# Kernel optimization log

Hardware: AMD Instinct MI355X
Metric: run time of the kernel (lower is better)

## Reference

```python
import jax, jax.numpy as jnp
import numpy as np
from jax import lax


def _l2n(t, eps=1e-12):
    n = jnp.sqrt(jnp.sum(t * t, axis=-1, keepdims=True))
    return t / jnp.maximum(n, eps)


def _ln(t, w, b, eps=1e-5):
    mu = jnp.mean(t, -1, keepdims=True)
    var = jnp.var(t, -1, keepdims=True)
    return (t - mu) / jnp.sqrt(var + eps) * w + b


def _unfold3(x):
    # nn.Unfold(kernel_size=3, padding=1, stride=1): [B,C,H,W] -> [B,C,9,H*W]
    B, C, H, W = x.shape
    xp = jnp.pad(x, ((0, 0), (0, 0), (1, 1), (1, 1)))
    pat = jnp.stack([xp[:, :, i:i + H, j:j + W] for i in range(3) for j in range(3)], axis=2)
    return pat.reshape(B, C, 9, H * W)


def _forward(x, norm1_w, norm1_b, q_w, q_b, kv_w, kv_b, temperature, query_embedding,
             learnable_tokens, learnable_bias, sr_w, sr_b, pln_w, pln_b, proj_w, proj_b,
             norm2_w, norm2_b, fc1_w, fc1_b, dw_w, dw_b, fc2_w, fc2_b):
    B, C, H, W = x.shape
    nh = temperature.shape[0]
    d = C // nh
    N = H * W
    K = 9  # local_len = window_size**2
    # norm1 (WithBias LayerNorm over channel dim, channels-last)
    y = _ln(x.reshape(B, C, N).transpose(0, 2, 1), norm1_w, norm1_b)  # [B,N,C]
    # ---- AggregatedAttention ----
    q = (y @ q_w.T + q_b).reshape(B, N, nh, d).transpose(0, 2, 1, 3)  # [B,h,N,d]
    qn = _l2n(q)
    qs = (qn + query_embedding) * jax.nn.softplus(temperature)
    kv = y @ kv_w.T + kv_b  # [B,N,2C]
    k_loc = _l2n(kv[..., :C].reshape(B, N, nh, d)).reshape(B, N, C)
    kvl = jnp.concatenate([k_loc, kv[..., C:]], -1).transpose(0, 2, 1).reshape(B, 2 * C, H, W)
    pat = _unfold3(kvl).reshape(B, 2 * nh, d, K, N).transpose(0, 1, 4, 2, 3)  # [B,2h,N,d,K]
    k_l, v_l = pat[:, :nh], pat[:, nh:]
    attn_local = jnp.einsum('bhnd,bhndk->bhnk', qs, k_l)  # [B,h,N,K]
    # pooled branch; sr_ratio=1 so adaptive_avg_pool2d is identity
    y4 = y.transpose(0, 2, 1).reshape(B, C, H, W)
    xp = jax.nn.gelu(jnp.einsum('oc,bchw->bohw', sr_w, y4) + sr_b[:, None, None], approximate=False)
    xp = _ln(xp.reshape(B, C, N).transpose(0, 2, 1), pln_w, pln_b)  # [B,pool_len,C]
    kvp = (xp @ kv_w.T + kv_b).reshape(B, N, 2 * nh, d).transpose(0, 2, 1, 3)
    k_p = _l2n(kvp[:, :nh])
    v_p = kvp[:, nh:]
    attn_pool = jnp.einsum('bhnd,bhmd->bhnm', qs, k_p)  # [B,h,N,pool_len]
    attn = jax.nn.softmax(jnp.concatenate([attn_local, attn_pool], -1), axis=-1)
    a_l, a_p = attn[..., :K], attn[..., K:]
    w_l = jnp.einsum('bhnd,hdk->bhnk', qn, learnable_tokens) + learnable_bias + a_l
    x_local = jnp.einsum('bhnk,bhndk->bhnd', w_l, v_l)
    x_pool = jnp.einsum('bhnm,bhmd->bhnd', a_p, v_p)
    xo = (x_local + x_pool).transpose(0, 2, 1, 3).reshape(B, N, C)
    # proj then raw torch-style reshape [B,N,C] -> [B,C,H,W] (memory reinterpretation)
    xo = (xo @ proj_w.T + proj_b).reshape(B, C, H, W)
    x = x + xo
    # ---- ConvolutionalGLU MLP ----
    hf = dw_b.shape[0]
    y2 = _ln(x.reshape(B, C, N).transpose(0, 2, 1), norm2_w, norm2_b).transpose(0, 2, 1).reshape(B, C, H, W)
    f1 = jnp.einsum('oc,bchw->bohw', fc1_w, y2) + fc1_b[:, None, None]
    a, v = f1[:, :hf], f1[:, hf:]
    dw = lax.conv_general_dilated(a, dw_w, (1, 1), ((1, 1), (1, 1)),
                                  feature_group_count=hf,
                                  dimension_numbers=('NCHW', 'OIHW', 'NCHW')) + dw_b[:, None, None]
    g = jax.nn.gelu(dw, approximate=False) * v
    out = jnp.einsum('oc,bchw->bohw', fc2_w, g) + fc2_b[:, None, None]
    return x + out


def setup_inputs() -> dict:
    key = jax.random.key(0)
    B, C, H, W = 2, 128, 56, 56
    nh, d, K = 4, 32, 9
    hf = int(2 * int(C * 4.0) / 3)  # 341
    ks = iter(jax.random.split(key, 16))
    rn = lambda shape, s=0.02: jax.random.normal(next(ks), shape, jnp.float32) * s
    return {
        'x': jax.random.normal(next(ks), (B, C, H, W), jnp.float32),
        'norm1_w': jnp.ones((C,), jnp.float32), 'norm1_b': jnp.zeros((C,), jnp.float32),
        'q_w': rn((C, C)), 'q_b': jnp.zeros((C,), jnp.float32),
        'kv_w': rn((2 * C, C)), 'kv_b': jnp.zeros((2 * C,), jnp.float32),
        'temperature': jnp.full((nh, 1, 1), float(np.log(np.exp(1.0 / 0.24) - 1.0)), jnp.float32),
        'query_embedding': rn((nh, 1, d)),
        'learnable_tokens': rn((nh, d, K)),
        'learnable_bias': jnp.zeros((nh, 1, K), jnp.float32),
        'sr_w': rn((C, C)), 'sr_b': jnp.zeros((C,), jnp.float32),
        'pln_w': jnp.ones((C,), jnp.float32), 'pln_b': jnp.zeros((C,), jnp.float32),
        'proj_w': rn((C, C)), 'proj_b': jnp.zeros((C,), jnp.float32),
        'norm2_w': jnp.ones((C,), jnp.float32), 'norm2_b': jnp.zeros((C,), jnp.float32),
        'fc1_w': rn((2 * hf, C)), 'fc1_b': jnp.zeros((2 * hf,), jnp.float32),
        'dw_w': rn((hf, 1, 3, 3)), 'dw_b': jnp.zeros((hf,), jnp.float32),
        'fc2_w': rn((C, hf)), 'fc2_b': jnp.zeros((C,), jnp.float32),
    }


def reference(x, norm1_w, norm1_b, q_w, q_b, kv_w, kv_b, temperature, query_embedding,
              learnable_tokens, learnable_bias, sr_w, sr_b, pln_w, pln_b, proj_w, proj_b,
              norm2_w, norm2_b, fc1_w, fc1_b, dw_w, dw_b, fc2_w, fc2_b):
    return _forward(x, norm1_w, norm1_b, q_w, q_b, kv_w, kv_b, temperature, query_embedding,
                    learnable_tokens, learnable_bias, sr_w, sr_b, pln_w, pln_b, proj_w, proj_b,
                    norm2_w, norm2_b, fc1_w, fc1_b, dw_w, dw_b, fc2_w, fc2_b)
```

## Files before the change

### kernel.cpp

```cpp
#include <hip/hip_runtime.h>
#include <hip/hip_bf16.h>

typedef __hip_bfloat16 bf16;
typedef _Float16 f16;
typedef short s8v __attribute__((ext_vector_type(8)));
typedef short s4v __attribute__((ext_vector_type(4)));
typedef float f4v __attribute__((ext_vector_type(4)));

#define DEVI __device__ __forceinline__

DEVI float cvt(float x){ return x; }
DEVI float cvt(bf16 x){ return __bfloat162float(x); }

DEVI void stg(float* p, float v){ *p = v; }
DEVI void stg(bf16* p, float v){ *p = __float2bfloat16(v); }

DEVI float gelu_exact(float x){
  return 0.5f*x*(1.0f + erff(x*0.70710678118654752440f));
}

constexpr int B_ = 2, C_ = 128, H_ = 56, W_ = 56, N_ = 3136, NH_ = 4, D_ = 32, HF_ = 341;
constexpr int ROWS_ = B_*N_;
constexpr int KF2 = 352;
constexpr int GQ_ = NH_*B_*N_;
constexpr int FW = 512;
constexpr int KSP = 8;
constexpr int SPLIT = 384;
constexpr float LOG2E = 1.4426950408889634f;
constexpr float E8L2  = 11.541560327111707f;

template<typename TX, typename TY, bool PLANES>
__global__ __launch_bounds__(256)
void ln_kernel(const TX* __restrict__ x, long xstr, const float* __restrict__ w,
               const float* __restrict__ bia, TY* __restrict__ y)
{
  int gid = blockIdx.x*4 + (threadIdx.x>>6);
  int lane = threadIdx.x & 63;
  int b = gid / N_, n = gid % N_;
  float v0, v1;
  if (PLANES){
    v0 = cvt(x[((long)b*C_ + lane     )*N_ + n]);
    v1 = cvt(x[((long)b*C_ + lane + 64)*N_ + n]);
  } else {
    v0 = cvt(x[(long)gid*xstr + lane     ]);
    v1 = cvt(x[(long)gid*xstr + lane + 64]);
  }
  float s = v0+v1, ss = v0*v0 + v1*v1;
  #pragma unroll
  for (int o=32;o>0;o>>=1){ s += __shfl_xor(s,o); ss += __shfl_xor(ss,o); }
  float mu  = s*(1.0f/128.0f);
  float var = fmaxf(ss*(1.0f/128.0f) - mu*mu, 0.f);
  float inv = rsqrtf(var + 1e-5f);
  stg(&y[(long)gid*C_ + lane     ], (v0-mu)*inv*w[lane     ] + bia[lane     ]);
  stg(&y[(long)gid*C_ + lane + 64], (v1-mu)*inv*w[lane + 64] + bia[lane + 64]);
}

__global__ __launch_bounds__(256)
void head_kernel(const float* __restrict__ q_w, const float* __restrict__ kv_w,
                 const float* __restrict__ sr_w, const float* __restrict__ proj_w,
                 const float* __restrict__ fc1_w, const float* __restrict__ fc2_w,
                 const float* __restrict__ q_b, const float* __restrict__ kv_b,
                 const float* __restrict__ sr_b,
                 bf16* __restrict__ out, float* __restrict__ bias_out,
                 const float* __restrict__ x_in, const float* __restrict__ n1w,
                 const float* __restrict__ n1b, bf16* __restrict__ y)
{
  if (blockIdx.x >= 839){
    int gid = (blockIdx.x - 839)*4 + (threadIdx.x>>6);
    int lane = threadIdx.x & 63;
    int b = gid / N_, n = gid % N_;
    float v0 = x_in[((long)b*C_ + lane     )*N_ + n];
    float v1 = x_in[((long)b*C_ + lane + 64)*N_ + n];
    float s = v0+v1, ss = v0*v0 + v1*v1;
    #pragma unroll
    for (int o=32;o>0;o>>=1){ s += __shfl_xor(s,o); ss += __shfl_xor(ss,o); }
    float mu  = s*(1.0f/128.0f);
    float var = fmaxf(ss*(1.0f/128.0f) - mu*mu, 0.f);
    float inv = rsqrtf(var + 1e-5f);
    y[(long)gid*C_ + lane     ] = __float2bfloat16((v0-mu)*inv*n1w[lane     ] + n1b[lane     ]);
    y[(long)gid*C_ + lane + 64] = __float2bfloat16((v1-mu)*inv*n1w[lane + 64] + n1b[lane + 64]);
    return;
  }
  int t = blockIdx.x*256 + threadIdx.x;
  if (t >= 214272){
    int i = t - 214272;
    if (i < 512){
      float bv = (i < 128) ? q_b[i] : (i < 384) ? kv_b[i-128] : sr_b[i-384];
      bias_out[i] = bv;
    }
    return;
  }
  float v;
  if      (t <  16384) v = q_w[t];
  else if (t <  49152) v = kv_w[t-16384];
  else if (t <  65536) v = sr_w[t-49152];
  else if (t <  81920) v = proj_w[t-65536];
  else if (t < 169216) v = fc1_w[t-81920];
  else {
    int i = t - 169216; int m = i / KF2, kp = i % KF2;
    v = (kp < HF_) ? fc2_w[m*HF_ + kp] : 0.f;
  }
  out[t] = __float2bfloat16(v);
}

template<int KT, int MODE, typename TC, int BM=64>
__global__ __launch_bounds__(256)
void gemm_mfma(const bf16* __restrict__ A, const bf16* __restrict__ B,
               const float* __restrict__ bias, const float* __restrict__ res,
               TC* __restrict__ Cm, int M, int Nn,
               long sA, long sB, long sC, long sR,
               const float* __restrict__ qe, const float* __restrict__ temp,
               bf16* __restrict__ aux0, bf16* __restrict__ aux1)
{
  A  += (long)blockIdx.z * sA;
  B  += (long)blockIdx.z * sB;
  Cm += (long)blockIdx.z * sC;
  if (res) res += (long)blockIdx.z * sR;
  int lane = threadIdx.x & 63, w = threadIdx.x >> 6;
  int m = lane & 15, quad = lane >> 4;
  int n0 = blockIdx.x*64, m0 = blockIdx.y*BM;
  int arow = m0 + w*16 + m;
  if (arow >= M) arow = M-1;
  const bf16* ap = A + (long)arow*KT + quad*8;
  const bf16* bp = B + (long)(n0 + m)*KT + quad*8;
  f4v acc[4];
  #pragma unroll
  for (int s=0;s<4;s++) acc[s] = (f4v){0.f,0.f,0.f,0.f};
  #pragma unroll
  for (int k0 = 0; k0 < KT; k0 += 32){
    s8v af = *(const s8v*)(ap + k0);
    #pragma unroll
    for (int s=0;s<4;s++){
      s8v bf = *(const s8v*)(bp + (long)s*16*KT + k0);
      acc[s] = __builtin_amdgcn_mfma_f32_16x16x32_bf16(af, bf, acc[s], 0, 0, 0);
    }
  }
  if ((MODE==6 || MODE==7) && blockIdx.x < 2){
    int hA = blockIdx.x*2, hB = hA+1;
    float spA = 0.f, spB = 0.f;
    if (MODE==6){
      spA = log1pf(expf(temp[hA])) * LOG2E;
      spB = log1pf(expf(temp[hB])) * LOG2E;
    }
    #pragma unroll
    for (int r=0;r<4;r++){
      float v4[4];
      #pragma unroll
      for (int s=0;s<4;s++) v4[s] = acc[s][r] + bias[n0 + s*16 + m];
      float ssA = v4[0]*v4[0] + v4[1]*v4[1];
      float ssB = v4[2]*v4[2] + v4[3]*v4[3];
      #pragma unroll
      for (int off=1; off<16; off<<=1){
        ssA += __shfl_xor(ssA, off);
        ssB += __shfl_xor(ssB, off);
      }
      float invA = 1.f/fmaxf(sqrtf(ssA), 1e-12f);
      float invB = 1.f/fmaxf(sqrtf(ssB), 1e-12f);
      int gm = m0 + w*16 + quad*4 + r;
      int b = gm / N_, n = gm % N_;
      #pragma unroll
      for (int s=0;s<4;s++){
        int h = (s<2) ? hA : hB;
        int d = (s&1)*16 + m;
        float v = v4[s] * ((s<2) ? invA : invB);
        if (MODE==6) v = (v + qe[h*D_ + d]) * ((s<2) ? spA : spB);
        aux0[((long)(b*NH_+h)*N_ + n)*D_ + d] = __float2bfloat16(v);
      }
    }
    return;
  }
  if (MODE==7){
    int gm0 = m0 + w*16 + quad*4;
    int b = gm0 / N_, nb = gm0 % N_;
    #pragma unroll
    for (int s=0;s<4;s++){
      int h = (blockIdx.x-2)*2 + (s>>1);
      int d = (s&1)*16 + m;
      bf16 p4[4];
      #pragma unroll
      for (int r=0;r<4;r++) p4[r] = __float2bfloat16(acc[s][r] + bias[n0 + s*16 + m]);
      *(s4v*)(aux1 + ((long)(b*NH_+h)*D_ + d)*N_ + nb) = *(const s4v*)p4;
    }
    return;
  }
  #pragma unroll
  for (int s=0;s<4;s++){
    int gn = n0 + s*16 + m;
    #pragma unroll
    for (int r=0;r<4;r++){
      int gm = m0 + w*16 + quad*4 + r;
      if (gm >= M) continue;
      float v = acc[s][r];
      if (MODE==1 || MODE==4 || MODE==6) v += bias[gn];
      else                               v += bias[gm];
      if (MODE==6 && gn >= 384) v = gelu_exact(v);
      if (MODE==4 || MODE==5) v += res[(long)gm*Nn + gn];
      stg(&Cm[(long)gm*Nn + gn], v);
    }
  }
}

__global__ __launch_bounds__(256)
void attn_part_kernel(const bf16* __restrict__ qs_, const bf16* __restrict__ kp_,
                      const bf16* __restrict__ vp_,
                      bf16* __restrict__ Op, float* __restrict__ Lp)
{
  int bh = blockIdx.y;
  int z  = blockIdx.z;
  int lane = threadIdx.x & 63;
  int w    = threadIdx.x >> 6;
  int m    = lane & 15, quad = lane >> 4;
  int base = blockIdx.x*256 + w*16;
  __shared__ float sm[4][640];
  float* Olds = sm[w];

  s8v af[4]; bool hasQ[4];
  #pragma unroll
  for (int ch=0; ch<4; ch++){
    int qq = base + ch*64;
    hasQ[ch] = (qq < N_);
    af[ch] = *(const s8v*)(qs_ + ((long)bh*N_ + (hasQ[ch] ? qq : base) + m)*D_ + quad*8);
  }
  const bf16* kpb = kp_ + (long)bh*N_*D_;
  const bf16* vpb = vp_ + (long)bh*D_*N_;
  int kperm = (m & 3) + 8*(m >> 2);
  f4v o0[4], o1[4];
  float l[4];
  #pragma unroll
  for (int ch=0; ch<4; ch++){
    o0[ch] = (f4v){0.f,0.f,0.f,0.f}; o1[ch] = (f4v){0.f,0.f,0.f,0.f};
    l[ch] = 0.f;
  }

  int tlo = z*SPLIT, thi = (z==KSP-1) ? N_ : tlo + SPLIT;
  for (int t0 = tlo; t0 < thi; t0 += 64){
    s8v kf[4];
    kf[0] = *(const s8v*)(kpb + (long)(t0 + kperm     )*D_ + quad*8);
    kf[1] = *(const s8v*)(kpb + (long)(t0 + kperm +  4)*D_ + quad*8);
    kf[2] = *(const s8v*)(kpb + (long)(t0 + kperm + 32)*D_ + quad*8);
    kf[3] = *(const s8v*)(kpb + (long)(t0 + kperm + 36)*D_ + quad*8);
    s8v vf0[2], vf1[2];
    #pragma unroll
    for (int c2=0;c2<2;c2++){
      vf0[c2] = *(const s8v*)(vpb + (long)(m     )*N_ + t0 + c2*32 + quad*8);
      vf1[c2] = *(const s8v*)(vpb + (long)(16 + m)*N_ + t0 + c2*32 + quad*8);
    }
    #pragma unroll
    for (int ch=0; ch<4; ch++){
      f4v c[4];
      #pragma unroll
      for (int s=0;s<4;s++){
        c[s] = (f4v){-E8L2, -E8L2, -E8L2, -E8L2};
        c[s] = __builtin_amdgcn_mfma_f32_16x16x32_bf16(kf[s], af[ch], c[s], 0, 0, 0);
      }
      bf16 p8a[8], p8b[8];
      float ls = 0.f;
      #pragma unroll
      for (int r=0;r<4;r++){
        float ea = __builtin_amdgcn_exp2f(c[0][r]);
        float eb = __builtin_amdgcn_exp2f(c[1][r]);
        float ec = __builtin_amdgcn_exp2f(c[2][r]);
        float ed = __builtin_amdgcn_exp2f(c[3][r]);
        ls += (ea+eb) + (ec+ed);
        p8a[r] = __float2bfloat16(ea); p8a[4+r] = __float2bfloat16(eb);
        p8b[r] = __float2bfloat16(ec); p8b[4+r] = __float2bfloat16(ed);
      }
      l[ch] += ls;
      s8v pa = *(const s8v*)p8a, pb = *(const s8v*)p8b;
      o0[ch] = __builtin_amdgcn_mfma_f32_16x16x32_bf16(pa, vf0[0], o0[ch], 0, 0, 0);
      o1[ch] = __builtin_amdgcn_mfma_f32_16x16x32_bf16(pa, vf1[0], o1[ch], 0, 0, 0);
      o0[ch] = __builtin_amdgcn_mfma_f32_16x16x32_bf16(pb, vf0[1], o0[ch], 0, 0, 0);
      o1[ch] = __builtin_amdgcn_mfma_f32_16x16x32_bf16(pb, vf1[1], o1[ch], 0, 0, 0);
    }
  }
  #pragma unroll
  for (int ch=0; ch<4; ch++){
    if (!hasQ[ch]) continue;
    float lr = l[ch];
    lr += __shfl_xor(lr, 16);
    lr += __shfl_xor(lr, 32);
    #pragma unroll
    for (int r=0;r<4;r++){
      Olds[(quad*4+r)*36 + m     ] = o0[ch][r];
      Olds[(quad*4+r)*36 + 16 + m] = o1[ch][r];
    }
    long gq = (long)bh*N_ + base + ch*64 + m;
    f4v ov0 = *(const f4v*)(Olds + m*36 + quad*8);
    f4v ov1 = *(const f4v*)(Olds + m*36 + quad*8 + 4);
    bf16 o8[8];
    #pragma unroll
    for (int j=0;j<4;j++){ o8[j] = __float2bfloat16(ov0[j]); o8[4+j] = __float2bfloat16(ov1[j]); }
    *(s8v*)(Op + ((long)z*GQ_ + gq)*32 + quad*8) = *(const s8v*)o8;
    if (quad == 0) Lp[(long)z*GQ_ + gq] = lr;
  }
}

__global__ __launch_bounds__(256)
void attn_combine_kernel(const bf16* __restrict__ Op, const float* __restrict__ Lp,
                         const bf16* __restrict__ qs_, const bf16* __restrict__ fused,
                         const float* __restrict__ qe, const float* __restrict__ temp,
                         const float* __restrict__ tokens, const float* __restrict__ tbias,
                         bf16* __restrict__ xo)
{
  int t  = blockIdx.x*256 + threadIdx.x;
  int gq = t >> 3;
  int l8 = t & 7;
  int d0 = l8*4;
  int n = gq % N_; int bh = gq / N_; int h = bh & 3; int b = bh >> 2;
  float out[4] = {0.f,0.f,0.f,0.f};
  #pragma unroll
  for (int z=0; z<KSP; z++){
    s4v o4 = *(const s4v*)(Op + ((long)z*GQ_ + gq)*32 + d0);
    #pragma unroll
    for (int j=0;j<4;j++) out[j] += cvt(((const bf16*)&o4)[j]);
  }
  float L = 0.f;
  for (int z=l8; z<KSP; z+=8) L += Lp[(long)z*GQ_ + gq];
  #pragma unroll
  for (int off=1; off<8; off<<=1) L += __shfl_xor(L, off);
  float q[4];
  {
    s4v q4 = *(const s4v*)(qs_ + (long)gq*D_ + d0);
    #pragma unroll
    for (int j=0;j<4;j++) q[j] = cvt(((const bf16*)&q4)[j]) * 0.6931471805599453f;
  }
  int hy = n / W_, wx = n % W_;
  const bf16* kvb = fused + (long)b*N_*FW + 128 + h*D_ + d0;
  float sl[9];
  #pragma unroll
  for (int k=0;k<9;k++){
    int di = k/3-1, dj = k%3-1;
    int yy = hy+di, xx = wx+dj;
    bool ok = (yy>=0 && yy<H_ && xx>=0 && xx<W_);
    float dot = 0.f, ss = 0.f;
    if (ok){
      s4v k4 = *(const s4v*)(kvb + (long)(yy*W_+xx)*FW);
      #pragma unroll
      for (int j=0;j<4;j++){
        float kk = cvt(((const bf16*)&k4)[j]);
        dot = fmaf(q[j], kk, dot);
        ss  = fmaf(kk, kk, ss);
      }
    }
    #pragma unroll
    for (int off=1; off<8; off<<=1){
      dot += __shfl_xor(dot, off);
      ss  += __shfl_xor(ss,  off);
    }
    sl[k] = ok ? dot / fmaxf(sqrtf(ss), 1e-12f) : 0.f;
  }
  #pragma unroll
  for (int k=0;k<9;k++) L += __expf(sl[k] - 8.f);
  float invL = 1.f/L;
  #pragma unroll
  for (int j=0;j<4;j++) out[j] *= invL;
  float sp = log1pf(expf(temp[h]));
  float invsp = 1.f/sp;
  float qn[4];
  #pragma unroll
  for (int j=0;j<4;j++) qn[j] = q[j]*invsp - qe[h*D_ + d0 + j];
  #pragma unroll
  for (int k=0;k<9;k++){
    float tok = 0.f;
    #pragma unroll
    for (int j=0;j<4;j++) tok = fmaf(qn[j], tokens[(h*D_ + d0 + j)*9 + k], tok);
    #pragma unroll
    for (int off=1; off<8; off<<=1) tok += __shfl_xor(tok, off);
    float wl = tok + tbias[h*9+k] + __expf(sl[k] - 8.f)*invL;
    int di = k/3-1, dj = k%3-1;
    int yy = hy+di, xx = wx+dj;
    if (yy>=0 && yy<H_ && xx>=0 && xx<W_){
      s4v v4 = *(const s4v*)(kvb + (long)(yy*W_+xx)*FW + 128);
      #pragma unroll
      for (int j=0;j<4;j++) out[j] = fmaf(wl, cvt(((const bf16*)&v4)[j]), out[j]);
    }
  }
  bf16 o4[4];
  #pragma unroll
  for (int j=0;j<4;j++) o4[j] = __float2bfloat16(out[j]);
  *(s4v*)(xo + ((long)(b*N_ + n))*C_ + h*D_ + d0) = *(const s4v*)o4;
}

__global__ __launch_bounds__(256)
void dwconv_kernel(const bf16* __restrict__ f1, const float* __restrict__ dww,
                   const float* __restrict__ dwb, bf16* __restrict__ g)
{
  int t = blockIdx.x*256 + threadIdx.x;
  if (t >= B_*N_*44) return;
  int b = t / (N_*44); int r = t - b*(N_*44);
  int n = r % N_, cg = r / N_;
  f1 += (long)b*2*HF_*N_;
  g  += (long)b*N_*KF2;
  int c0 = cg*8;
  int hy = n / W_, wx = n % W_;
  bf16 o8[8];
  #pragma unroll
  for (int j=0;j<8;j++){
    int c = c0 + j;
    float val = 0.f;
    if (c < HF_){
      const bf16* ap = f1 + (long)c*N_;
      float s = dwb[c];
      #pragma unroll
      for (int di=-1; di<=1; di++)
        #pragma unroll
        for (int dj=-1; dj<=1; dj++){
          int yy = hy+di, xx = wx+dj;
          if (yy>=0 && yy<H_ && xx>=0 && xx<W_)
            s = fmaf(dww[c*9 + (di+1)*3 + (dj+1)], cvt(ap[yy*W_+xx]), s);
        }
      val = gelu_exact(s) * cvt(f1[(long)(HF_+c)*N_ + n]);
    }
    o8[j] = __float2bfloat16(val);
  }
  *(s8v*)(g + (long)n*KF2 + c0) = *(const s8v*)o8;
}

extern "C" void kernel_launch(void* const* d_in, const int* in_sizes, int n_in,
                              void* d_out, int out_size, void* d_ws, size_t ws_size,
                              hipStream_t stream)
{
  (void)in_sizes; (void)n_in; (void)out_size; (void)ws_size;
  const float* x_in      = (const float*)d_in[0];
  const float* norm1_w   = (const float*)d_in[1];
  const float* norm1_b   = (const float*)d_in[2];
  const float* q_w       = (const float*)d_in[3];
  const float* q_b       = (const float*)d_in[4];
  const float* kv_w      = (const float*)d_in[5];
  const float* kv_b      = (const float*)d_in[6];
  const float* temp      = (const float*)d_in[7];
  const float* qe        = (const float*)d_in[8];
  const float* tokens    = (const float*)d_in[9];
  const float* tbias     = (const float*)d_in[10];
  const float* sr_w      = (const float*)d_in[11];
  const float* sr_b      = (const float*)d_in[12];
  const float* pln_w     = (const float*)d_in[13];
  const float* pln_b     = (const float*)d_in[14];
  const float* proj_w    = (const float*)d_in[15];
  const float* proj_b    = (const float*)d_in[16];
  const float* norm2_w   = (const float*)d_in[17];
  const float* norm2_b   = (const float*)d_in[18];
  const float* fc1_w     = (const float*)d_in[19];
  const float* fc1_b     = (const float*)d_in[20];
  const float* dw_w      = (const float*)d_in[21];
  const float* dw_b      = (const float*)d_in[22];
  const float* fc2_w     = (const float*)d_in[23];
  const float* fc2_b     = (const float*)d_in[24];

  char* w8 = (char*)d_ws;
  bf16*  fused   = (bf16*)(w8 + 0);
  float* x2      = (float*)(w8 + 0);
  bf16*  y2      = (bf16*)(w8 + 3211264);
  bf16*  f1b     = (bf16*)(w8 + 4816896);
  bf16*  qs      = (bf16*)(w8 + 6422528);
  bf16*  xp      = (bf16*)(w8 + 8028160);
  bf16*  k_p     = (bf16*)(w8 + 9633792);
  bf16*  v_p     = (bf16*)(w8 + 11239424);
  bf16*  Opart   = (bf16*)(w8 + 13045056);
  bf16*  g_rows  = (bf16*)(w8 + 32312640);
  bf16*  wbase   = (bf16*)(w8 + 36728128);
  float* fbias   = (float*)(w8 + 37156672);
  bf16*  y       = f1b;
  bf16*  xo      = (bf16*)d_out;
  float* Lpart   = (float*)((char*)d_out + 1605632);
  bf16*  proj_wb = wbase + 65536;
  bf16*  fc1_wb  = wbase + 81920;
  bf16*  fc2_wb  = wbase + 169216;

  head_kernel<<<839 + ROWS_/4, 256, 0, stream>>>(
      q_w, kv_w, sr_w, proj_w, fc1_w, fc2_w, q_b, kv_b, sr_b, wbase, fbias,
      x_in, norm1_w, norm1_b, y);
  gemm_mfma<128, 6, bf16><<<dim3(8,98), 256, 0, stream>>>(
      y, wbase, fbias, nullptr, fused, ROWS_, FW, 0,0,0,0, qe, temp, qs, nullptr);
  ln_kernel<bf16, bf16, false><<<ROWS_/4, 256, 0, stream>>>(fused + 384, FW, pln_w, pln_b, xp);
  gemm_mfma<128, 7, bf16><<<dim3(4,98), 256, 0, stream>>>(
      xp, wbase + 16384, kv_b, nullptr, (bf16*)nullptr, ROWS_, 256, 0,0,0,0,
      nullptr, nullptr, k_p, v_p);
  attn_part_kernel<<<dim3(13,8,KSP), 256, 0, stream>>>(qs, k_p, v_p, Opart, Lpart);
  attn_combine_kernel<<<GQ_*8/256, 256, 0, stream>>>(Opart, Lpart, qs, fused,
                                                     qe, temp, tokens, tbias, xo);
  gemm_mfma<128, 4, float, 32><<<dim3(2,196), 128, 0, stream>>>(
      xo, proj_wb, proj_b, x_in, x2, ROWS_, 128, 0,0,0,0, nullptr, nullptr, nullptr, nullptr);
  ln_kernel<float, bf16, true><<<ROWS_/4, 256, 0, stream>>>(x2, 0, norm2_w, norm2_b, y2);
  gemm_mfma<128, 3, bf16><<<dim3(49,11,B_), 256, 0, stream>>>(
      fc1_wb, y2, fc1_b, nullptr, f1b, 2*HF_, N_,
      0, (long)N_*C_, (long)2*HF_*N_, 0, nullptr, nullptr, nullptr, nullptr);
  dwconv_kernel<<<(B_*N_*44+255)/256, 256, 0, stream>>>(f1b, dw_w, dw_b, g_rows);
  gemm_mfma<KF2, 5, float, 32><<<dim3(49,4,B_), 128, 0, stream>>>(
      fc2_wb, g_rows, fc2_b, x2, (float*)d_out, C_, N_,
      0, (long)N_*KF2, (long)C_*N_, (long)C_*N_, nullptr, nullptr, nullptr, nullptr);
}
```

Before: 245.6 us.

## Fuse pooled LayerNorm into kv GEMM and double-buffer K/V loads in attention

The separate LayerNorm kernel over the pooled branch is removed. Each MODE-7 GEMM lane now loads its A row from the fused buffer with stride FW, computes the row mean and variance with cross-lane shuffles, and normalizes in registers before the MFMA loop. The attention partial kernel also gets a two-stage register double buffer that loads the next K/V tile while the current one is computed. This saves a launch and an intermediate round trip through memory, but raises register pressure and recomputes the LayerNorm for every column block.

```diff
diff --git a/kernel.cpp b/kernel.cpp
--- a/kernel.cpp
+++ b/kernel.cpp
@@ -2,7 +2,6 @@
 #include <hip/hip_bf16.h>
 
 typedef __hip_bfloat16 bf16;
-typedef _Float16 f16;
 typedef short s8v __attribute__((ext_vector_type(8)));
 typedef short s4v __attribute__((ext_vector_type(4)));
 typedef float f4v __attribute__((ext_vector_type(4)));
@@ -103,7 +102,7 @@
   out[t] = __float2bfloat16(v);
 }
 
-template<int KT, int MODE, typename TC, int BM=64>
+template<int KT, int MODE, typename TC, int BM=64, int LDA=KT>
 __global__ __launch_bounds__(256)
 void gemm_mfma(const bf16* __restrict__ A, const bf16* __restrict__ B,
                const float* __restrict__ bias, const float* __restrict__ res,
@@ -121,14 +120,41 @@
   int n0 = blockIdx.x*64, m0 = blockIdx.y*BM;
   int arow = m0 + w*16 + m;
   if (arow >= M) arow = M-1;
-  const bf16* ap = A + (long)arow*KT + quad*8;
+  const bf16* ap = A + (long)arow*LDA + quad*8;
   const bf16* bp = B + (long)(n0 + m)*KT + quad*8;
+  s8v a4[KT/32];
+  if (MODE==7){
+    float s=0.f, ssum=0.f;
+    #pragma unroll
+    for (int i=0;i<KT/32;i++){
+      a4[i] = *(const s8v*)(ap + i*32);
+      #pragma unroll
+      for (int j=0;j<8;j++){
+        float v = cvt(((const bf16*)&a4[i])[j]);
+        s += v; ssum = fmaf(v,v,ssum);
+      }
+    }
+    s    += __shfl_xor(s,16);    s    += __shfl_xor(s,32);
+    ssum += __shfl_xor(ssum,16); ssum += __shfl_xor(ssum,32);
+    float mu  = s*(1.0f/128.0f);
+    float var = fmaxf(ssum*(1.0f/128.0f) - mu*mu, 0.f);
+    float inv = rsqrtf(var + 1e-5f);
+    #pragma unroll
+    for (int i=0;i<KT/32;i++){
+      #pragma unroll
+      for (int j=0;j<8;j++){
+        int c = i*32 + quad*8 + j;
+        float v = cvt(((const bf16*)&a4[i])[j]);
+        ((bf16*)&a4[i])[j] = __float2bfloat16((v-mu)*inv*qe[c] + temp[c]);
+      }
+    }
+  }
   f4v acc[4];
   #pragma unroll
   for (int s=0;s<4;s++) acc[s] = (f4v){0.f,0.f,0.f,0.f};
   #pragma unroll
   for (int k0 = 0; k0 < KT; k0 += 32){
-    s8v af = *(const s8v*)(ap + k0);
+    s8v af = (MODE==7) ? a4[k0/32] : *(const s8v*)(ap + k0);
     #pragma unroll
     for (int s=0;s<4;s++){
       s8v bf = *(const s8v*)(bp + (long)s*16*KT + k0);
@@ -232,19 +258,17 @@
     l[ch] = 0.f;
   }
 
-  int tlo = z*SPLIT, thi = (z==KSP-1) ? N_ : tlo + SPLIT;
-  for (int t0 = tlo; t0 < thi; t0 += 64){
-    s8v kf[4];
-    kf[0] = *(const s8v*)(kpb + (long)(t0 + kperm     )*D_ + quad*8);
-    kf[1] = *(const s8v*)(kpb + (long)(t0 + kperm +  4)*D_ + quad*8);
-    kf[2] = *(const s8v*)(kpb + (long)(t0 + kperm + 32)*D_ + quad*8);
-    kf[3] = *(const s8v*)(kpb + (long)(t0 + kperm + 36)*D_ + quad*8);
-    s8v vf0[2], vf1[2];
-    #pragma unroll
-    for (int c2=0;c2<2;c2++){
-      vf0[c2] = *(const s8v*)(vpb + (long)(m     )*N_ + t0 + c2*32 + quad*8);
-      vf1[c2] = *(const s8v*)(vpb + (long)(16 + m)*N_ + t0 + c2*32 + quad*8);
-    }
+  auto loadKV = [&](s8v* kf, s8v* vf, int t){
+    kf[0] = *(const s8v*)(kpb + (long)(t + kperm     )*D_ + quad*8);
+    kf[1] = *(const s8v*)(kpb + (long)(t + kperm +  4)*D_ + quad*8);
+    kf[2] = *(const s8v*)(kpb + (long)(t + kperm + 32)*D_ + quad*8);
+    kf[3] = *(const s8v*)(kpb + (long)(t + kperm + 36)*D_ + quad*8);
+    vf[0] = *(const s8v*)(vpb + (long)(m     )*N_ + t      + quad*8);
+    vf[1] = *(const s8v*)(vpb + (long)(16 + m)*N_ + t      + quad*8);
+    vf[2] = *(const s8v*)(vpb + (long)(m     )*N_ + t + 32 + quad*8);
+    vf[3] = *(const s8v*)(vpb + (long)(16 + m)*N_ + t + 32 + quad*8);
+  };
+  auto compute = [&](const s8v* kf, const s8v* vf){
     #pragma unroll
     for (int ch=0; ch<4; ch++){
       f4v c[4];
@@ -267,11 +291,26 @@
       }
       l[ch] += ls;
       s8v pa = *(const s8v*)p8a, pb = *(const s8v*)p8b;
-      o0[ch] = __builtin_amdgcn_mfma_f32_16x16x32_bf16(pa, vf0[0], o0[ch], 0, 0, 0);
-      o1[ch] = __builtin_amdgcn_mfma_f32_16x16x32_bf16(pa, vf1[0], o1[ch], 0, 0, 0);
-      o0[ch] = __builtin_amdgcn_mfma_f32_16x16x32_bf16(pb, vf0[1], o0[ch], 0, 0, 0);
-      o1[ch] = __builtin_amdgcn_mfma_f32_16x16x32_bf16(pb, vf1[1], o1[ch], 0, 0, 0);
-    }
+      o0[ch] = __builtin_amdgcn_mfma_f32_16x16x32_bf16(pa, vf[0], o0[ch], 0, 0, 0);
+      o1[ch] = __builtin_amdgcn_mfma_f32_16x16x32_bf16(pa, vf[1], o1[ch], 0, 0, 0);
+      o0[ch] = __builtin_amdgcn_mfma_f32_16x16x32_bf16(pb, vf[2], o0[ch], 0, 0, 0);
+      o1[ch] = __builtin_amdgcn_mfma_f32_16x16x32_bf16(pb, vf[3], o1[ch], 0, 0, 0);
+    }
+  };
+
+  int tlo = z*SPLIT, thi = (z==KSP-1) ? N_ : tlo + SPLIT;
+  s8v kfA[4], vfA[4], kfB[4], vfB[4];
+  int t0 = tlo;
+  loadKV(kfA, vfA, t0);
+  for (;;){
+    if (t0 + 64 < thi) loadKV(kfB, vfB, t0 + 64);
+    compute(kfA, vfA);
+    t0 += 64;
+    if (t0 >= thi) break;
+    if (t0 + 64 < thi) loadKV(kfA, vfA, t0 + 64);
+    compute(kfB, vfB);
+    t0 += 64;
+    if (t0 >= thi) break;
   }
   #pragma unroll
   for (int ch=0; ch<4; ch++){
@@ -453,7 +492,6 @@
   bf16*  y2      = (bf16*)(w8 + 3211264);
   bf16*  f1b     = (bf16*)(w8 + 4816896);
   bf16*  qs      = (bf16*)(w8 + 6422528);
-  bf16*  xp      = (bf16*)(w8 + 8028160);
   bf16*  k_p     = (bf16*)(w8 + 9633792);
   bf16*  v_p     = (bf16*)(w8 + 11239424);
   bf16*  Opart   = (bf16*)(w8 + 13045056);
@@ -472,10 +510,9 @@
       x_in, norm1_w, norm1_b, y);
   gemm_mfma<128, 6, bf16><<<dim3(8,98), 256, 0, stream>>>(
       y, wbase, fbias, nullptr, fused, ROWS_, FW, 0,0,0,0, qe, temp, qs, nullptr);
-  ln_kernel<bf16, bf16, false><<<ROWS_/4, 256, 0, stream>>>(fused + 384, FW, pln_w, pln_b, xp);
-  gemm_mfma<128, 7, bf16><<<dim3(4,98), 256, 0, stream>>>(
-      xp, wbase + 16384, kv_b, nullptr, (bf16*)nullptr, ROWS_, 256, 0,0,0,0,
-      nullptr, nullptr, k_p, v_p);
+  gemm_mfma<128, 7, bf16, 64, FW><<<dim3(4,98), 256, 0, stream>>>(
+      fused + 384, wbase + 16384, kv_b, nullptr, (bf16*)nullptr, ROWS_, 256, 0,0,0,0,
+      pln_w, pln_b, k_p, v_p);
   attn_part_kernel<<<dim3(13,8,KSP), 256, 0, stream>>>(qs, k_p, v_p, Opart, Lpart);
   attn_combine_kernel<<<GQ_*8/256, 256, 0, stream>>>(Opart, Lpart, qs, fused,
                                                      qe, temp, tokens, tbias, xo);
```

After: 243.1 us. Within noise of the previous version (-1.0%).
